# Kernel optimization log

Hardware: AMD Instinct MI355X
Metric: run time of the kernel (lower is better)

Reference implementation:

```python
import jax, jax.numpy as jnp
import numpy as np

CHANNELS = 64
K = 3
STRIDE = 1
GROUP_CHANNELS = 2
GROUPS = CHANNELS // GROUP_CHANNELS  # 32
RED = 4
PAD = (K - 1) // 2


def setup_inputs() -> dict:
    key = jax.random.key(0)
    ks = jax.random.split(key, 6)
    x = jax.random.normal(ks[0], (8, CHANNELS, 128, 128), dtype=jnp.float32)
    w1 = jax.random.normal(ks[1], (CHANNELS // RED, CHANNELS), dtype=jnp.float32) * 0.05
    b1 = jax.random.normal(ks[2], (CHANNELS // RED,), dtype=jnp.float32) * 0.05
    prelu_a = jnp.full((1,), 0.25, dtype=jnp.float32)
    w2 = jax.random.normal(ks[3], (K * K * GROUPS, CHANNELS // RED), dtype=jnp.float32) * 0.05
    b2 = jax.random.normal(ks[4], (K * K * GROUPS,), dtype=jnp.float32) * 0.05
    return {"x": x, "w1": w1, "b1": b1, "prelu_a": prelu_a, "w2": w2, "b2": b2}


def reference(x, w1, b1, prelu_a, w2, b2):
    # stride == 1: no avgpool
    # 1x1 conv -> PReLU -> 1x1 conv to generate per-pixel kernels
    t = jnp.einsum('bchw,oc->bohw', x, w1) + b1[None, :, None, None]
    t = jnp.where(t >= 0, t, prelu_a[0] * t)  # PReLU, single shared slope
    weight = jnp.einsum('bchw,oc->bohw', t, w2) + b2[None, :, None, None]
    b, _, h, w = weight.shape
    # (b, groups, 1, k^2, h, w)
    weight = weight.reshape(b, GROUPS, 1, K * K, h, w)
    # unfold: im2col with padding 1, stride 1; channel-major (c, kh, kw) ordering like torch.nn.Unfold
    xp = jnp.pad(x, ((0, 0), (0, 0), (PAD, PAD), (PAD, PAD)))
    patches = jnp.stack(
        [xp[:, :, i:i + h, j:j + w] for i in range(K) for j in range(K)], axis=2
    )  # (b, c, k^2, h, w)
    patches = patches.reshape(b, GROUPS, GROUP_CHANNELS, K * K, h, w)
    out = (weight * patches).sum(axis=3).reshape(b, CHANNELS, h, w)
    return out
```

## Files before the change

### kernel.cpp

```cpp
#include <hip/hip_runtime.h>

#define NPIX (128 * 128)
#define CH 64
#define RMID 16
#define GROUPS 32
#define KK 9

__global__ __launch_bounds__(512, 4) void involution_fused(
    const float* __restrict__ x,
    const float* __restrict__ w1,
    const float* __restrict__ b1,
    const float* __restrict__ prelu_a,
    const float* __restrict__ w2,
    const float* __restrict__ b2,
    float* __restrict__ out)
{
    __shared__ float tl[256 * 17];

    const int px    = threadIdx.x & 255;
    const int layer = threadIdx.x >> 8;

    const int blk = blockIdx.x;
    const int bq  = blk >> 6;
    const int hp  = blk & 63;
    const int hq  = 2 * hp + (px >> 7);
    const int wq  = px & 127;
    const int p   = hq * 128 + wq;

    const float* xb = x + (size_t)bq * CH * NPIX;

    const int r0 = 8 * layer;
    float t8[8];
#pragma unroll
    for (int r = 0; r < 8; ++r) t8[r] = b1[r0 + r];

#pragma unroll 8
    for (int c = 0; c < CH; ++c) {
        const float xv = xb[(size_t)c * NPIX + p];
#pragma unroll
        for (int r = 0; r < 8; ++r)
            t8[r] = fmaf(w1[(r0 + r) * CH + c], xv, t8[r]);
    }
    const float a = prelu_a[0];
#pragma unroll
    for (int r = 0; r < 8; ++r) {
        const float v = t8[r];
        tl[px * 17 + r0 + r] = (v >= 0.f) ? v : a * v;
    }
    __syncthreads();

    float tr[RMID];
#pragma unroll
    for (int r = 0; r < RMID; ++r) tr[r] = tl[px * 17 + r];

    int   qb[KK];
    float msk[KK];
#pragma unroll
    for (int i = 0; i < 3; ++i) {
#pragma unroll
        for (int j = 0; j < 3; ++j) {
            const int k  = i * 3 + j;
            const int dh = i - 1, dw = j - 1;
            const bool okk = ((unsigned)(hq + dh) < 128u) && ((unsigned)(wq + dw) < 128u);
            qb[k]  = 4 * (okk ? (p + dh * 128 + dw) : p);
            msk[k] = okk ? 1.f : 0.f;
        }
    }

    const char* xbc = (const char*)xb;
    char*       obc = (char*)(out + (size_t)bq * CH * NPIX);
    const int   pb  = 4 * p;

#pragma unroll 4
    for (int gi = 0; gi < 16; ++gi) {
        const int g = __builtin_amdgcn_readfirstlane(16 * layer + gi);

        const char* c0 = xbc + (size_t)(2 * g) * NPIX * 4;
        const char* c1 = c0 + (size_t)NPIX * 4;

        float p0[KK], p1[KK];
#pragma unroll
        for (int k = 0; k < KK; ++k) {
            p0[k] = *(const float*)(c0 + qb[k]);
            p1[k] = *(const float*)(c1 + qb[k]);
        }

        float wg[KK];
#pragma unroll
        for (int k = 0; k < KK; ++k) {
            float acc = b2[g * KK + k];
            const float* w2r = w2 + (g * KK + k) * RMID;
#pragma unroll
            for (int r = 0; r < RMID; ++r)
                acc = fmaf(w2r[r], tr[r], acc);
            wg[k] = acc * msk[k];
        }

        float o0 = 0.f, o1 = 0.f;
#pragma unroll
        for (int k = 0; k < KK; ++k) {
            o0 = fmaf(wg[k], p0[k], o0);
            o1 = fmaf(wg[k], p1[k], o1);
        }
        *(float*)(obc + (size_t)(2 * g)     * NPIX * 4 + pb) = o0;
        *(float*)(obc + (size_t)(2 * g + 1) * NPIX * 4 + pb) = o1;
    }
}

extern "C" void kernel_launch(void* const* d_in, const int* in_sizes, int n_in,
                              void* d_out, int out_size, void* d_ws, size_t ws_size,
                              hipStream_t stream)
{
    const float* x  = (const float*)d_in[0];
    const float* w1 = (const float*)d_in[1];
    const float* b1 = (const float*)d_in[2];
    const float* pa = (const float*)d_in[3];
    const float* w2 = (const float*)d_in[4];
    const float* b2 = (const float*)d_in[5];
    float* out = (float*)d_out;

    const int nblocks = 8 * 64;
    hipLaunchKernelGGL(involution_fused, dim3(nblocks), dim3(512), 0, stream,
                       x, w1, b1, pa, w2, b2, out);
}
```

Baseline: 133.0 us.

## Split work to one row per block with four channel layers and interior fast path

```diff
diff --git a/kernel.cpp b/kernel.cpp
--- a/kernel.cpp
+++ b/kernel.cpp
@@ -5,84 +5,34 @@
 #define RMID 16
 #define GROUPS 32
 #define KK 9
+#define PLANE_B (NPIX * 4)
 
-__global__ __launch_bounds__(512, 4) void involution_fused(
-    const float* __restrict__ x,
-    const float* __restrict__ w1,
-    const float* __restrict__ b1,
-    const float* __restrict__ prelu_a,
-    const float* __restrict__ w2,
-    const float* __restrict__ b2,
-    float* __restrict__ out)
+
+template<bool INTERIOR>
+__device__ __forceinline__ void run_groups(
+    const char* __restrict__ xbc, char* __restrict__ obc,
+    const float* __restrict__ w2, const float* __restrict__ b2,
+    const float* tr, int layer, int pb,
+    int cneg, int cpos, float mneg, float mpos,
+    const int* roa, const float* rm)
 {
-    __shared__ float tl[256 * 17];
-
-    const int px    = threadIdx.x & 255;
-    const int layer = threadIdx.x >> 8;
-
-    const int blk = blockIdx.x;
-    const int bq  = blk >> 6;
-    const int hp  = blk & 63;
-    const int hq  = 2 * hp + (px >> 7);
-    const int wq  = px & 127;
-    const int p   = hq * 128 + wq;
-
-    const float* xb = x + (size_t)bq * CH * NPIX;
-
-    const int r0 = 8 * layer;
-    float t8[8];
-#pragma unroll
-    for (int r = 0; r < 8; ++r) t8[r] = b1[r0 + r];
-
-#pragma unroll 8
-    for (int c = 0; c < CH; ++c) {
-        const float xv = xb[(size_t)c * NPIX + p];
-#pragma unroll
-        for (int r = 0; r < 8; ++r)
-            t8[r] = fmaf(w1[(r0 + r) * CH + c], xv, t8[r]);
-    }
-    const float a = prelu_a[0];
-#pragma unroll
-    for (int r = 0; r < 8; ++r) {
-        const float v = t8[r];
-        tl[px * 17 + r0 + r] = (v >= 0.f) ? v : a * v;
-    }
-    __syncthreads();
-
-    float tr[RMID];
-#pragma unroll
-    for (int r = 0; r < RMID; ++r) tr[r] = tl[px * 17 + r];
-
-    int   qb[KK];
-    float msk[KK];
-#pragma unroll
-    for (int i = 0; i < 3; ++i) {
-#pragma unroll
-        for (int j = 0; j < 3; ++j) {
-            const int k  = i * 3 + j;
-            const int dh = i - 1, dw = j - 1;
-            const bool okk = ((unsigned)(hq + dh) < 128u) && ((unsigned)(wq + dw) < 128u);
-            qb[k]  = 4 * (okk ? (p + dh * 128 + dw) : p);
-            msk[k] = okk ? 1.f : 0.f;
-        }
-    }
-
-    const char* xbc = (const char*)xb;
-    char*       obc = (char*)(out + (size_t)bq * CH * NPIX);
-    const int   pb  = 4 * p;
-
-#pragma unroll 4
-    for (int gi = 0; gi < 16; ++gi) {
-        const int g = __builtin_amdgcn_readfirstlane(16 * layer + gi);
-
-        const char* c0 = xbc + (size_t)(2 * g) * NPIX * 4;
-        const char* c1 = c0 + (size_t)NPIX * 4;
+#pragma unroll 2
+    for (int gi = 0; gi < 8; ++gi) {
+        const int g = __builtin_amdgcn_readfirstlane(layer * 8 + gi);
+        const char* c0 = xbc + (size_t)(2 * g) * PLANE_B;
+        const char* c1 = c0 + PLANE_B;
 
         float p0[KK], p1[KK];
 #pragma unroll
-        for (int k = 0; k < KK; ++k) {
-            p0[k] = *(const float*)(c0 + qb[k]);
-            p1[k] = *(const float*)(c1 + qb[k]);
+        for (int i = 0; i < 3; ++i) {
+#pragma unroll
+            for (int j = 0; j < 3; ++j) {
+                const int k    = i * 3 + j;
+                const int voff = (j == 0) ? cneg : (j == 2) ? cpos : pb;
+                const int ro   = INTERIOR ? (i - 1) * 512 : roa[i];
+                p0[k] = *(const float*)(c0 + (size_t)(voff + ro));
+                p1[k] = *(const float*)(c1 + (size_t)(voff + ro));
+            }
         }
 
         float wg[KK];
@@ -93,7 +43,14 @@
 #pragma unroll
             for (int r = 0; r < RMID; ++r)
                 acc = fmaf(w2r[r], tr[r], acc);
-            wg[k] = acc * msk[k];
+            wg[k] = acc;
+        }
+#pragma unroll
+        for (int i = 0; i < 3; ++i) {
+            const float rmv = INTERIOR ? 1.f : rm[i];
+            wg[i * 3 + 0] *= mneg * rmv;
+            wg[i * 3 + 1] *= rmv;
+            wg[i * 3 + 2] *= mpos * rmv;
         }
 
         float o0 = 0.f, o1 = 0.f;
@@ -102,8 +59,73 @@
             o0 = fmaf(wg[k], p0[k], o0);
             o1 = fmaf(wg[k], p1[k], o1);
         }
-        *(float*)(obc + (size_t)(2 * g)     * NPIX * 4 + pb) = o0;
-        *(float*)(obc + (size_t)(2 * g + 1) * NPIX * 4 + pb) = o1;
+        *(float*)(obc + (size_t)(2 * g) * PLANE_B + pb)       = o0;
+        *(float*)(obc + (size_t)(2 * g + 1) * PLANE_B + pb)   = o1;
+    }
+}
+
+__global__ __launch_bounds__(512, 6) void involution_fused(
+    const float* __restrict__ x,
+    const float* __restrict__ w1,
+    const float* __restrict__ b1,
+    const float* __restrict__ prelu_a,
+    const float* __restrict__ w2,
+    const float* __restrict__ b2,
+    float* __restrict__ out)
+{
+    __shared__ float tl[128 * 17];
+
+    const int px    = threadIdx.x & 127;
+    const int layer = threadIdx.x >> 7;
+
+    const int blk = blockIdx.x;
+    const int bq  = blk >> 7;
+    const int hq  = blk & 127;
+    const int p   = hq * 128 + px;
+
+    const float* xb = x + (size_t)bq * CH * NPIX;
+
+    const int r0 = 4 * layer;
+    float t4[4];
+#pragma unroll
+    for (int r = 0; r < 4; ++r) t4[r] = b1[r0 + r];
+
+#pragma unroll 16
+    for (int c = 0; c < CH; ++c) {
+        const float xv = xb[(size_t)c * NPIX + p];
+#pragma unroll
+        for (int r = 0; r < 4; ++r)
+            t4[r] = fmaf(w1[(r0 + r) * CH + c], xv, t4[r]);
+    }
+    const float a = prelu_a[0];
+#pragma unroll
+    for (int r = 0; r < 4; ++r) {
+        const float v = t4[r];
+        tl[px * 17 + r0 + r] = (v >= 0.f) ? v : a * v;
+    }
+    __syncthreads();
+
+    float tr[RMID];
+#pragma unroll
+    for (int r = 0; r < RMID; ++r) tr[r] = tl[px * 17 + r];
+
+    const int   pb   = 4 * p;
+    const int   cneg = (px > 0)   ? pb - 4 : pb;
+    const int   cpos = (px < 127) ? pb + 4 : pb;
+    const float mneg = (px > 0)   ? 1.f : 0.f;
+    const float mpos = (px < 127) ? 1.f : 0.f;
+
+    const char* xbc = (const char*)xb;
+    char*       obc = (char*)(out + (size_t)bq * CH * NPIX);
+
+    if (hq >= 1 && hq <= 126) {
+        run_groups<true>(xbc, obc, w2, b2, tr, layer, pb,
+                         cneg, cpos, mneg, mpos, nullptr, nullptr);
+    } else {
+        int   roa[3] = { (hq > 0) ? -512 : 0, 0, (hq < 127) ? 512 : 0 };
+        float rm[3]  = { (hq > 0) ? 1.f : 0.f, 1.f, (hq < 127) ? 1.f : 0.f };
+        run_groups<false>(xbc, obc, w2, b2, tr, layer, pb,
+                          cneg, cpos, mneg, mpos, roa, rm);
     }
 }
 
@@ -119,7 +141,7 @@
     const float* b2 = (const float*)d_in[5];
     float* out = (float*)d_out;
 
-    const int nblocks = 8 * 64;
+    const int nblocks = 8 * 128;
     hipLaunchKernelGGL(involution_fused, dim3(nblocks), dim3(512), 0, stream,
                        x, w1, b1, pa, w2, b2, out);
 }
```

After: 140.4 us. 5.6% more time.
